# Optimization experiments

Measured on AMD Instinct MI355X. Metric: run time of the kernel, lower is better.

The kernel has to match this reference:

```python
import jax, jax.numpy as jnp
import numpy as np

VOCAB, INPUT, HIDDEN = 100, 512, 1024
BATCH, SEQ = 64, 512


def setup_inputs() -> dict:
    key = jax.random.key(0)
    ks = jax.random.split(key, 12)
    s = 0.02
    inp = {
        "X": jax.random.randint(ks[0], (BATCH, SEQ), 0, VOCAB, dtype=jnp.int64 if jax.config.jax_enable_x64 else jnp.int32),
        "h0": jnp.zeros((BATCH, HIDDEN), jnp.float32),
        "c0": jnp.zeros((BATCH, HIDDEN), jnp.float32),
        "emb": jax.random.normal(ks[1], (VOCAB, INPUT), jnp.float32) * s,
        "Wf_w": jax.random.normal(ks[2], (HIDDEN, INPUT + HIDDEN), jnp.float32) * s,
        "Wf_b": jnp.zeros((HIDDEN,), jnp.float32),
        "Wi_w": jax.random.normal(ks[3], (HIDDEN, INPUT + HIDDEN), jnp.float32) * s,
        "Wi_b": jnp.zeros((HIDDEN,), jnp.float32),
        "Wo_w": jax.random.normal(ks[4], (HIDDEN, INPUT + HIDDEN), jnp.float32) * s,
        "Wo_b": jnp.zeros((HIDDEN,), jnp.float32),
        "Wg_w": jax.random.normal(ks[5], (HIDDEN, INPUT + HIDDEN), jnp.float32) * s,
        "Wg_b": jnp.zeros((HIDDEN,), jnp.float32),
    }
    return inp


def reference(X, h0, c0, emb, Wf_w, Wf_b, Wi_w, Wi_b, Wo_w, Wo_b, Wg_w, Wg_b):
    # Fuse the 4 gate Linears into one GEMM (same math, concatenated rows).
    W = jnp.concatenate([Wf_w, Wi_w, Wo_w, Wg_w], axis=0)   # [4H, I+H]
    b = jnp.concatenate([Wf_b, Wi_b, Wo_b, Wg_b], axis=0)   # [4H]
    H = Wf_w.shape[0]

    xs = emb[X]                       # [B, S, I]
    xs = jnp.swapaxes(xs, 0, 1)       # [S, B, I] for scan over time

    def step(carry, x_t):
        h, c = carry
        combined = jnp.concatenate([x_t, h], axis=1)          # [B, I+H]
        z = combined @ W.T + b                                # [B, 4H]
        ft = jax.nn.sigmoid(z[:, 0*H:1*H])
        it = jax.nn.sigmoid(z[:, 1*H:2*H])
        ot = jax.nn.sigmoid(z[:, 2*H:3*H])
        gt = jnp.tanh(z[:, 3*H:4*H])
        c_t = ft * c + it * gt
        h_t = ot * jnp.tanh(c_t)
        return (h_t, c_t), h_t

    (h_f, c_f), hs = jax.lax.scan(step, (h0, c0), xs)
    latent = jnp.swapaxes(hs, 0, 1)   # [B, S, H]
    return latent, (h_f, c_f)
```

## Files before the change

kernel.cpp:

```cpp
#include <hip/hip_runtime.h>


typedef _Float16 f16x8 __attribute__((ext_vector_type(8)));
typedef float    f32x4 __attribute__((ext_vector_type(4)));
typedef unsigned int u32x4 __attribute__((ext_vector_type(4)));

#define VOCABN 100
#define SENTW 0xFEFEFEFEu

__global__ void k0_zxtable(const float* __restrict__ emb,
                           const float* __restrict__ Wf, const float* __restrict__ bf,
                           const float* __restrict__ Wi, const float* __restrict__ bi,
                           const float* __restrict__ Wo, const float* __restrict__ bo,
                           const float* __restrict__ Wg, const float* __restrict__ bg_,
                           float* __restrict__ zx) {
  const int bid = blockIdx.x;
  const int g = bid >> 6, chunk = bid & 63;
  const float* W = (g==0)?Wf:(g==1)?Wi:(g==2)?Wo:Wg;
  const float* B = (g==0)?bf:(g==1)?bi:(g==2)?bo:bg_;
  __shared__ float Wl[16][516];
  const int tid = threadIdx.x;
  for (int i = tid; i < 2048; i += 256) {
    int r = i >> 7, c4 = i & 127;
    float4 v = *(const float4*)&W[(size_t)(chunk*16 + r)*1536 + c4*4];
    Wl[r][c4*4+0]=v.x; Wl[r][c4*4+1]=v.y; Wl[r][c4*4+2]=v.z; Wl[r][c4*4+3]=v.w;
  }
  __syncthreads();
  const int u = tid & 15, vi = tid >> 4;
  for (int v0 = 0; v0 < VOCABN; v0 += 16) {
    int v = v0 + vi;
    if (v < VOCABN) {
      const float* er = emb + (size_t)v*512;
      float acc = 0.f;
      #pragma unroll 8
      for (int k = 0; k < 512; k++) acc += er[k]*Wl[u][k];
      zx[(size_t)v*4096 + g*1024 + chunk*16 + u] = acc + B[chunk*16 + u];
    }
  }
}

__global__ void k1_prep(const float* __restrict__ Wf, const float* __restrict__ Wi,
                        const float* __restrict__ Wo, const float* __restrict__ Wg,
                        const float* __restrict__ h0,
                        _Float16* __restrict__ Whh, _Float16* __restrict__ hstage) {
  const int bid = blockIdx.x, tid = threadIdx.x;
  if (bid < 1024) {
    #pragma unroll
    for (int i = 0; i < 4; i++) {
      int F = bid*1024 + i*256 + tid;
      int g = F >> 18;
      int rem = F & ((1<<18)-1);
      int n = rem >> 8, k4 = rem & 255;
      const float* W = (g==0)?Wf:(g==1)?Wi:(g==2)?Wo:Wg;
      float4 v = *(const float4*)&W[(size_t)n*1536 + 512 + k4*4];
      _Float16 h4[4] = {(_Float16)v.x,(_Float16)v.y,(_Float16)v.z,(_Float16)v.w};
      *(unsigned long long*)&Whh[((size_t)g<<20) + (n<<10) + (k4<<2)] =
          *(unsigned long long*)h4;
    }
  } else {
    int j = bid - 1024;
    int base = j*1024 + tid*4;
    float4 v = *(const float4*)&h0[base];
    _Float16 h4[4] = {(_Float16)v.x,(_Float16)v.y,(_Float16)v.z,(_Float16)v.w};
    *(unsigned long long*)&hstage[7*65536 + base] = *(unsigned long long*)h4;
  }
}

__global__ __launch_bounds__(512, 1) void lstm_main(
    const int* __restrict__ X, const float* __restrict__ c0,
    const float* __restrict__ zx, const _Float16* __restrict__ Whh,
    _Float16* __restrict__ hstage, float* out)
{
  const int bid = blockIdx.x;
  const int bg  = bid >> 5;
  const int js  = bid & 31;
  const int tid = threadIdx.x;
  const int w   = tid >> 6;
  const int l   = tid & 63;
  const int lm = l & 15, lh = l >> 4;

  __shared__ alignas(16) _Float16 hs[16384];
  __shared__ float zsh[8][132];

  f16x8 bw[32];
  {
    const _Float16* wp = Whh + ((size_t)(w>>1)<<20)
                       + ((size_t)(js*32 + (w&1)*16 + lm)<<10) + (lh<<3);
    #pragma unroll
    for (int kk = 0; kk < 32; kk++) {
      asm volatile("global_load_dwordx4 %0, %1, off"
                   : "=&v"(bw[kk]) : "v"(wp + kk*32));
    }
    asm volatile("s_waitcnt vmcnt(0)");
    __builtin_amdgcn_sched_barrier(0);
  }

  const int kk  = 4*w + lh;
  const int srw = l & 7;
  const int kp  = (l >> 3) & 1;
  const unsigned sgoff = (unsigned)((bg*8 + srw)*2048 + kk*64 + kp*32);
  char* lw = (char*)hs + kk*1024 + kp*512 + srw*16;
  const char* hb = (const char*)hs + (l << 4);

  const int b = (tid >> 5) & 7, u = tid & 31;
  const int brow = bg*8 + b, ucol = js*32 + u;
  float c = 0.f, hkeep = 0.f;
  const int* Xr = nullptr;
  if (tid < 256) {
    c = c0[(size_t)brow*1024 + ucol];
    Xr = X + (size_t)brow*512;
  }
  float* latp = out + (size_t)brow*512*1024 + ucol;
  const unsigned pboff = (unsigned)(brow*2048 + (js*32 + (u & 24))*2);

  float zc0=0.f, zc1=0.f, zc2=0.f, zc3=0.f;
  if (tid < 256) {
    int xv = Xr[0];
    const float* p = zx + (size_t)xv*4096 + ucol;
    zc0 = p[0]; zc1 = p[1024]; zc2 = p[2048]; zc3 = p[3072];
  }

  for (int t = 0; t < 512; t++) {
    float zn0=0.f, zn1=0.f, zn2=0.f, zn3=0.f;
    if (tid < 256 && t < 511) {
      int xv = Xr[t+1];
      const float* p = zx + (size_t)xv*4096 + ucol;
      zn0 = p[0]; zn1 = p[1024]; zn2 = p[2048]; zn3 = p[3072];
    }

    u32x4 va, vb;
    {
      const char* sb = (const char*)hstage + ((unsigned)((t+7)&7) << 17) + sgoff;
      int spin = 0;
      for (;;) {
        asm volatile(
          "global_load_dwordx4 %0, %2, off sc1\n\t"
          "global_load_dwordx4 %1, %2, off offset:16 sc1\n\t"
          "s_waitcnt vmcnt(0)"
          : "=&v"(va), "=&v"(vb) : "v"(sb));
        bool bad = (va.x==SENTW)|(va.y==SENTW)|(va.z==SENTW)|(va.w==SENTW)
                 | (vb.x==SENTW)|(vb.y==SENTW)|(vb.z==SENTW)|(vb.w==SENTW);
        if (!bad || ++spin > (1<<18)) break;
      }
    }
    if (t > 0 && tid < 256)
      __builtin_nontemporal_store(hkeep, latp + (size_t)(t-1)*1024);
    *(u32x4*)(lw)       = va;
    *(u32x4*)(lw + 256) = vb;
    __syncthreads();

    f32x4 a0={0,0,0,0}, a1={0,0,0,0}, a2={0,0,0,0}, a3={0,0,0,0};
    #pragma unroll
    for (int k2 = 0; k2 < 32; k2 += 4) {
      f16x8 x0 = *(const f16x8*)(hb + (k2+0)*1024);
      f16x8 x1 = *(const f16x8*)(hb + (k2+1)*1024);
      f16x8 x2 = *(const f16x8*)(hb + (k2+2)*1024);
      f16x8 x3 = *(const f16x8*)(hb + (k2+3)*1024);
      a0 = __builtin_amdgcn_mfma_f32_16x16x32_f16(x0, bw[k2+0], a0, 0, 0, 0);
      a1 = __builtin_amdgcn_mfma_f32_16x16x32_f16(x1, bw[k2+1], a1, 0, 0, 0);
      a2 = __builtin_amdgcn_mfma_f32_16x16x32_f16(x2, bw[k2+2], a2, 0, 0, 0);
      a3 = __builtin_amdgcn_mfma_f32_16x16x32_f16(x3, bw[k2+3], a3, 0, 0, 0);
    }
    f32x4 z4 = (a0 + a1) + (a2 + a3);
    if (lh < 2) {
      #pragma unroll
      for (int r4 = 0; r4 < 4; r4++)
        zsh[lh*4 + r4][(w>>1)*32 + (w&1)*16 + lm] = z4[r4];
    }
    __syncthreads();

    if (tid < 256) {
      float zf = zsh[b][u]      + zc0;
      float zi = zsh[b][32+u]   + zc1;
      float zo = zsh[b][64+u]   + zc2;
      float zg = zsh[b][96+u]   + zc3;
      float fg = 1.f/(1.f + __expf(-zf));
      float ig = 1.f/(1.f + __expf(-zi));
      float og = 1.f/(1.f + __expf(-zo));
      float e2g = __expf(2.f*zg);
      float gg = 1.f - 2.f/(e2g + 1.f);
      c = fg*c + ig*gg;
      float e2c = __expf(2.f*c);
      hkeep = og*(1.f - 2.f/(e2c + 1.f));

      if (t < 511) {
        unsigned hu = (unsigned)__builtin_bit_cast(unsigned short, (_Float16)hkeep);
        unsigned o1 = (unsigned)__shfl_xor((int)hu, 1);
        unsigned d  = (l & 1) ? ((o1 & 0xffffu) | (hu << 16))
                              : ((hu & 0xffffu) | (o1 << 16));
        unsigned o2 = (unsigned)__shfl_xor((int)d, 2);
        unsigned q0 = (l & 2) ? o2 : d;
        unsigned q1 = (l & 2) ? d : o2;
        unsigned o3a = (unsigned)__shfl_xor((int)q0, 4);
        unsigned o3b = (unsigned)__shfl_xor((int)q1, 4);
        u32x4 pk;
        if (l & 4) { pk[0]=o3a; pk[1]=o3b; pk[2]=q0; pk[3]=q1; }
        else       { pk[0]=q0;  pk[1]=q1;  pk[2]=o3a; pk[3]=o3b; }
        if ((l & 7) == 0) {
          char* pb = (char*)hstage + ((unsigned)( t   &7) << 17) + pboff;
          char* rb = (char*)hstage + ((unsigned)((t+4)&7) << 17) + pboff;
          u32x4 sv; sv[0]=SENTW; sv[1]=SENTW; sv[2]=SENTW; sv[3]=SENTW;
          asm volatile(
            "global_store_dwordx4 %0, %1, off sc1\n\t"
            "global_store_dwordx4 %2, %3, off sc1"
            :: "v"(rb), "v"(sv), "v"(pb), "v"(pk) : "memory");
        }
      }
    }
    zc0 = zn0; zc1 = zn1; zc2 = zn2; zc3 = zn3;
  }

  if (tid < 256) {
    __builtin_nontemporal_store(hkeep, latp + (size_t)511*1024);
    out[33554432 + ((size_t)brow<<10) + ucol] = hkeep;
    out[33619968 + ((size_t)brow<<10) + ucol] = c;
  }
}

extern "C" void kernel_launch(void* const* d_in, const int* in_sizes, int n_in,
                              void* d_out, int out_size, void* d_ws, size_t ws_size,
                              hipStream_t stream) {
  const int*   X   = (const int*)  d_in[0];
  const float* h0  = (const float*)d_in[1];
  const float* c0  = (const float*)d_in[2];
  const float* emb = (const float*)d_in[3];
  const float* Wf  = (const float*)d_in[4];  const float* bf = (const float*)d_in[5];
  const float* Wi  = (const float*)d_in[6];  const float* bi = (const float*)d_in[7];
  const float* Wo  = (const float*)d_in[8];  const float* bo = (const float*)d_in[9];
  const float* Wg  = (const float*)d_in[10]; const float* bg = (const float*)d_in[11];
  float* out = (float*)d_out;

  char* ws = (char*)d_ws;
  float*    zx     = (float*)   ws;
  _Float16* Whh    = (_Float16*)(ws + 1638400);
  _Float16* hstage = (_Float16*)(ws + 1638400 + 8388608);

  hipMemsetAsync(hstage, 0xFE, 8*131072, stream);
  k0_zxtable<<<256, 256, 0, stream>>>(emb, Wf, bf, Wi, bi, Wo, bo, Wg, bg, zx);
  k1_prep<<<1088, 256, 0, stream>>>(Wf, Wi, Wo, Wg, h0, Whh, hstage);
  lstm_main<<<256, 512, 0, stream>>>(X, c0, zx, Whh, hstage, out);
}
```

Measured before the change: 1.749 ms.

## Replace sentinel-polling h exchange with per-step flags and full-history staging slots

Cross-block synchronization of the hidden state changes from spinning on sentinel words in an 8-slot ring to per-timestep, per-producer flag words. Each block waits for the flag of its producer block, then reads h. When the workspace is big enough, each timestep gets its own slot, so the h loads can skip the sc1 cache bypass and no sentinel reset stores are needed. The block index mapping is also swapped so the batch group varies fastest, and the latent store moves into the step itself. In exchange, every step now ends with an extra vmcnt wait and a block barrier before the flag store, and correctness relies on flag visibility ordering.

```diff
diff --git a/kernel.cpp b/kernel.cpp
--- a/kernel.cpp
+++ b/kernel.cpp
@@ -6,7 +6,6 @@
 typedef unsigned int u32x4 __attribute__((ext_vector_type(4)));
 
 #define VOCABN 100
-#define SENTW 0xFEFEFEFEu
 
 __global__ void k0_zxtable(const float* __restrict__ emb,
                            const float* __restrict__ Wf, const float* __restrict__ bf,
@@ -42,7 +41,7 @@
 __global__ void k1_prep(const float* __restrict__ Wf, const float* __restrict__ Wi,
                         const float* __restrict__ Wo, const float* __restrict__ Wg,
                         const float* __restrict__ h0,
-                        _Float16* __restrict__ Whh, _Float16* __restrict__ hstage) {
+                        _Float16* __restrict__ Whh, _Float16* __restrict__ h0slot) {
   const int bid = blockIdx.x, tid = threadIdx.x;
   if (bid < 1024) {
     #pragma unroll
@@ -62,18 +61,20 @@
     int base = j*1024 + tid*4;
     float4 v = *(const float4*)&h0[base];
     _Float16 h4[4] = {(_Float16)v.x,(_Float16)v.y,(_Float16)v.z,(_Float16)v.w};
-    *(unsigned long long*)&hstage[7*65536 + base] = *(unsigned long long*)h4;
-  }
-}
-
+    *(unsigned long long*)&h0slot[base] = *(unsigned long long*)h4;
+  }
+}
+
+template<bool CACHED>
 __global__ __launch_bounds__(512, 1) void lstm_main(
     const int* __restrict__ X, const float* __restrict__ c0,
     const float* __restrict__ zx, const _Float16* __restrict__ Whh,
-    _Float16* __restrict__ hstage, float* out)
+    _Float16* __restrict__ hstage, int* __restrict__ flags, float* out)
 {
+  constexpr unsigned SLOT_MASK = CACHED ? 511u : 7u;
   const int bid = blockIdx.x;
-  const int bg  = bid >> 5;
-  const int js  = bid & 31;
+  const int bg  = bid & 7;
+  const int js  = bid >> 3;
   const int tid = threadIdx.x;
   const int w   = tid >> 6;
   const int l   = tid & 63;
@@ -130,21 +131,30 @@
 
     u32x4 va, vb;
     {
-      const char* sb = (const char*)hstage + ((unsigned)((t+7)&7) << 17) + sgoff;
-      int spin = 0;
-      for (;;) {
+      if (t > 0) {
+        const int* fp = flags + (t-1)*256 + bg*32 + kk;
+        int f, spin = 0;
+        do {
+          asm volatile("global_load_dword %0, %1, off sc1\n\t"
+                       "s_waitcnt vmcnt(0)" : "=v"(f) : "v"(fp));
+        } while (f == 0 && ++spin < (1<<16));
+      }
+      const char* sb = (const char*)hstage
+                     + ((size_t)((unsigned)(t+511) & SLOT_MASK) << 17) + sgoff;
+      if constexpr (CACHED) {
+        asm volatile(
+          "global_load_dwordx4 %0, %2, off\n\t"
+          "global_load_dwordx4 %1, %2, off offset:16\n\t"
+          "s_waitcnt vmcnt(0)"
+          : "=&v"(va), "=&v"(vb) : "v"(sb));
+      } else {
         asm volatile(
           "global_load_dwordx4 %0, %2, off sc1\n\t"
           "global_load_dwordx4 %1, %2, off offset:16 sc1\n\t"
           "s_waitcnt vmcnt(0)"
           : "=&v"(va), "=&v"(vb) : "v"(sb));
-        bool bad = (va.x==SENTW)|(va.y==SENTW)|(va.z==SENTW)|(va.w==SENTW)
-                 | (vb.x==SENTW)|(vb.y==SENTW)|(vb.z==SENTW)|(vb.w==SENTW);
-        if (!bad || ++spin > (1<<18)) break;
       }
     }
-    if (t > 0 && tid < 256)
-      __builtin_nontemporal_store(hkeep, latp + (size_t)(t-1)*1024);
     *(u32x4*)(lw)       = va;
     *(u32x4*)(lw + 256) = vb;
     __syncthreads();
@@ -182,6 +192,8 @@
       c = fg*c + ig*gg;
       float e2c = __expf(2.f*c);
       hkeep = og*(1.f - 2.f/(e2c + 1.f));
+
+      __builtin_nontemporal_store(hkeep, latp + (size_t)t*1024);
 
       if (t < 511) {
         unsigned hu = (unsigned)__builtin_bit_cast(unsigned short, (_Float16)hkeep);
@@ -197,21 +209,24 @@
         if (l & 4) { pk[0]=o3a; pk[1]=o3b; pk[2]=q0; pk[3]=q1; }
         else       { pk[0]=q0;  pk[1]=q1;  pk[2]=o3a; pk[3]=o3b; }
         if ((l & 7) == 0) {
-          char* pb = (char*)hstage + ((unsigned)( t   &7) << 17) + pboff;
-          char* rb = (char*)hstage + ((unsigned)((t+4)&7) << 17) + pboff;
-          u32x4 sv; sv[0]=SENTW; sv[1]=SENTW; sv[2]=SENTW; sv[3]=SENTW;
-          asm volatile(
-            "global_store_dwordx4 %0, %1, off sc1\n\t"
-            "global_store_dwordx4 %2, %3, off sc1"
-            :: "v"(rb), "v"(sv), "v"(pb), "v"(pk) : "memory");
+          char* pb = (char*)hstage + ((size_t)((unsigned)t & SLOT_MASK) << 17) + pboff;
+          asm volatile("global_store_dwordx4 %0, %1, off sc1"
+                       :: "v"(pb), "v"(pk) : "memory");
         }
       }
     }
+
+    asm volatile("s_waitcnt vmcnt(0)");
+    __syncthreads();
+    if (tid == 0 && t < 511) {
+      const int one = 1;
+      asm volatile("global_store_dword %0, %1, off sc1"
+                   :: "v"(flags + t*256 + bg*32 + js), "v"(one) : "memory");
+    }
     zc0 = zn0; zc1 = zn1; zc2 = zn2; zc3 = zn3;
   }
 
   if (tid < 256) {
-    __builtin_nontemporal_store(hkeep, latp + (size_t)511*1024);
     out[33554432 + ((size_t)brow<<10) + ucol] = hkeep;
     out[33619968 + ((size_t)brow<<10) + ucol] = c;
   }
@@ -231,12 +246,22 @@
   float* out = (float*)d_out;
 
   char* ws = (char*)d_ws;
-  float*    zx     = (float*)   ws;
-  _Float16* Whh    = (_Float16*)(ws + 1638400);
-  _Float16* hstage = (_Float16*)(ws + 1638400 + 8388608);
-
-  hipMemsetAsync(hstage, 0xFE, 8*131072, stream);
+  const size_t base = 1638400 + 8388608;
+  float*    zx  = (float*)   ws;
+  _Float16* Whh = (_Float16*)(ws + 1638400);
+
+  const size_t need_big = base + (size_t)512*131072 + 524288;
+  const bool   big      = ws_size >= need_big;
+  const size_t nslots   = big ? 512 : 8;
+  _Float16* hstage = (_Float16*)(ws + base);
+  int*      flags  = (int*)    (ws + base + nslots*131072);
+  _Float16* h0slot = hstage + (big ? (size_t)511*65536 : (size_t)7*65536);
+
+  hipMemsetAsync(flags, 0, 524288, stream);
   k0_zxtable<<<256, 256, 0, stream>>>(emb, Wf, bf, Wi, bi, Wo, bo, Wg, bg, zx);
-  k1_prep<<<1088, 256, 0, stream>>>(Wf, Wi, Wo, Wg, h0, Whh, hstage);
-  lstm_main<<<256, 512, 0, stream>>>(X, c0, zx, Whh, hstage, out);
-}
+  k1_prep<<<1088, 256, 0, stream>>>(Wf, Wi, Wo, Wg, h0, Whh, h0slot);
+  if (big)
+    lstm_main<true><<<256, 512, 0, stream>>>(X, c0, zx, Whh, hstage, flags, out);
+  else
+    lstm_main<false><<<256, 512, 0, stream>>>(X, c0, zx, Whh, hstage, flags, out);
+}
```

Result: faster. 1.700 ms (-2.8%).
